# Kernel tuning notes

Hardware: AMD Instinct MI355X
Metric: run time of the kernel (lower is better)

The kernel has to match this reference:

```python
import jax, jax.numpy as jnp
import numpy as np

EPS = 1e-6
DIM, HEADS, HEAD_DIM, FFN = 1024, 16, 64, 4096
B, S = 2, 2048


def layer_norm(x, g, b):
    m = jnp.mean(x, axis=-1, keepdims=True)
    v = jnp.mean(jnp.square(x - m), axis=-1, keepdims=True)
    return (x - m) * jax.lax.rsqrt(v + EPS) * g + b


def apply_rope(x, cos, sin):
    # x: (b, h, s, d); cos/sin: (s, d) broadcast over b, h
    x1, x2 = jnp.split(x, 2, axis=-1)
    rot = jnp.concatenate([-x2, x1], axis=-1)
    return x * cos + rot * sin


def setup_inputs() -> dict:
    key = jax.random.key(0)
    ks = jax.random.split(key, 24)
    sc_in = 1.0 / np.sqrt(DIM)
    sc_ffn = 1.0 / np.sqrt(FFN)
    inp = {
        "x": jax.random.normal(ks[0], (B, S, DIM), jnp.float32),
        "rope_cos": jax.random.uniform(ks[1], (S, HEAD_DIM), jnp.float32),
        "rope_sin": jax.random.uniform(ks[2], (S, HEAD_DIM), jnp.float32),
        "w_qkv": jax.random.normal(ks[3], (3 * DIM, DIM), jnp.float32) * sc_in,
        "b_qkv": jnp.zeros((3 * DIM,), jnp.float32),
        "w_out": jax.random.normal(ks[4], (DIM, DIM), jnp.float32) * sc_in,
        "b_out": jnp.zeros((DIM,), jnp.float32),
        "qn_g": jnp.ones((DIM,), jnp.float32),
        "qn_b": jnp.zeros((DIM,), jnp.float32),
        "kn_g": jnp.ones((DIM,), jnp.float32),
        "kn_b": jnp.zeros((DIM,), jnp.float32),
        "ln1_g": jnp.ones((DIM,), jnp.float32),
        "ln1_b": jnp.zeros((DIM,), jnp.float32),
        "ln2_g": jnp.ones((DIM,), jnp.float32),
        "ln2_b": jnp.zeros((DIM,), jnp.float32),
        "w1": jax.random.normal(ks[5], (FFN, DIM), jnp.float32) * sc_in,
        "b1": jnp.zeros((FFN,), jnp.float32),
        "w2": jax.random.normal(ks[6], (DIM, FFN), jnp.float32) * sc_ffn,
        "b2": jnp.zeros((DIM,), jnp.float32),
        "w3": jax.random.normal(ks[7], (FFN, DIM), jnp.float32) * sc_in,
        "b3": jnp.zeros((FFN,), jnp.float32),
    }
    return inp


def reference(x, rope_cos, rope_sin, w_qkv, b_qkv, w_out, b_out,
              qn_g, qn_b, kn_g, kn_b, ln1_g, ln1_b, ln2_g, ln2_b,
              w1, b1, w2, b2, w3, b3):
    bs, s, d = x.shape
    # --- pre-norm self-attention ---
    h = layer_norm(x, ln1_g, ln1_b)
    qkv = h @ w_qkv.T + b_qkv                      # (b, s, 3d)
    q, k, v = jnp.split(qkv, 3, axis=-1)
    q = layer_norm(q, qn_g, qn_b)                  # QK-norm over full dim
    k = layer_norm(k, kn_g, kn_b)
    # (b, s, d) -> (b, h, s, hd)
    q = q.reshape(bs, s, HEADS, HEAD_DIM).transpose(0, 2, 1, 3)
    k = k.reshape(bs, s, HEADS, HEAD_DIM).transpose(0, 2, 1, 3)
    v = v.reshape(bs, s, HEADS, HEAD_DIM).transpose(0, 2, 1, 3)
    q = apply_rope(q, rope_cos, rope_sin)
    k = apply_rope(k, rope_cos, rope_sin)
    scale = 1.0 / np.sqrt(HEAD_DIM)
    scores = jnp.einsum('bhqd,bhkd->bhqk', q, k) * scale
    probs = jax.nn.softmax(scores, axis=-1)
    attn = jnp.einsum('bhqk,bhkd->bhqd', probs, v)
    attn = attn.transpose(0, 2, 1, 3).reshape(bs, s, d)
    x = x + (attn @ w_out.T + b_out)
    # --- pre-norm SwiGLU FFN ---
    h2 = layer_norm(x, ln2_g, ln2_b)
    ffn = (jax.nn.silu(h2 @ w1.T + b1) * (h2 @ w3.T + b3)) @ w2.T + b2
    return x + ffn
```

## Files before the change

kernel.cpp:

```cpp
#include <hip/hip_runtime.h>
#include <hip/hip_bf16.h>


typedef __bf16 bf16_t;
typedef bf16_t bf16x8 __attribute__((ext_vector_type(8)));
typedef bf16_t bf16x4 __attribute__((ext_vector_type(4)));
typedef float  f32x4  __attribute__((ext_vector_type(4)));
typedef float  f32x16 __attribute__((ext_vector_type(16)));

#define DIM   1024
#define HEADS 16
#define HD    64
#define FFND  4096
#define NB    2
#define SEQ   2048
#define NTOK  (NB * SEQ)

#define GLOAD16(gp, lp) __builtin_amdgcn_global_load_lds( \
    (const __attribute__((address_space(1))) void*)(gp),  \
    (__attribute__((address_space(3))) void*)(lp), 16, 0, 0)

#define CVTPK(lo, hi_) ({ unsigned r_;                                        \
  asm("v_cvt_pk_bf16_f32 %0, %1, %2" : "=v"(r_) : "v"(lo), "v"(hi_)); r_; })
#define PLSWAP(a, b) asm("v_permlane32_swap_b32 %0, %1" : "+v"(a), "+v"(b))

#define F2B_S0 786432
#define F2B_S1 262144
#define F2B_S2 1048576
#define F2B_S3 1048576
#define F2B_S4 1048576
#define F2B_C1 (F2B_S0)
#define F2B_C2 (F2B_C1 + F2B_S1)
#define F2B_C3 (F2B_C2 + F2B_S2)
#define F2B_C4 (F2B_C3 + F2B_S3)
#define F2B_N  (F2B_C4 + F2B_S4)

__global__ void f2bf_all_kernel(const float* __restrict__ s0, const float* __restrict__ s1,
                                const float* __restrict__ s2, const float* __restrict__ s3,
                                const float* __restrict__ s4,
                                bf16_t* __restrict__ d0, bf16_t* __restrict__ d1,
                                bf16_t* __restrict__ d2, bf16_t* __restrict__ d3,
                                bf16_t* __restrict__ d4) {
  int idx = blockIdx.x * blockDim.x + threadIdx.x;
  int stride = gridDim.x * blockDim.x;
  for (; idx < F2B_N; idx += stride) {
    const float* src; bf16_t* dst; int i;
    if (idx < F2B_C1)      { src = s0; dst = d0; i = idx; }
    else if (idx < F2B_C2) { src = s1; dst = d1; i = idx - F2B_C1; }
    else if (idx < F2B_C3) { src = s2; dst = d2; i = idx - F2B_C2; }
    else if (idx < F2B_C4) { src = s3; dst = d3; i = idx - F2B_C3; }
    else                   { src = s4; dst = d4; i = idx - F2B_C4; }
    float4 v = reinterpret_cast<const float4*>(src)[i];
    bf16x4 o;
    o[0] = (bf16_t)v.x; o[1] = (bf16_t)v.y; o[2] = (bf16_t)v.z; o[3] = (bf16_t)v.w;
    reinterpret_cast<bf16x4*>(dst)[i] = o;
  }
}

__global__ __launch_bounds__(256) void ln_kernel(
    const float* __restrict__ x, const float* __restrict__ g,
    const float* __restrict__ b, bf16_t* __restrict__ out) {
  int t = blockIdx.x;
  int i = threadIdx.x;
  float4 v = reinterpret_cast<const float4*>(x + (size_t)t * DIM)[i];
  float s  = v.x + v.y + v.z + v.w;
  float s2 = v.x * v.x + v.y * v.y + v.z * v.z + v.w * v.w;
#pragma unroll
  for (int off = 32; off > 0; off >>= 1) {
    s  += __shfl_down(s, off, 64);
    s2 += __shfl_down(s2, off, 64);
  }
  __shared__ float red[2][4];
  int wid = i >> 6, lane = i & 63;
  if (lane == 0) { red[0][wid] = s; red[1][wid] = s2; }
  __syncthreads();
  float S  = red[0][0] + red[0][1] + red[0][2] + red[0][3];
  float S2 = red[1][0] + red[1][1] + red[1][2] + red[1][3];
  float mean = S * (1.0f / DIM);
  float var  = S2 * (1.0f / DIM) - mean * mean;
  float r = rsqrtf(var + 1e-6f);
  float vv[4] = {v.x, v.y, v.z, v.w};
  bf16x4 o;
#pragma unroll
  for (int j = 0; j < 4; ++j) {
    int d = i * 4 + j;
    o[j] = (bf16_t)((vv[j] - mean) * r * g[d] + b[d]);
  }
  *reinterpret_cast<bf16x4*>(out + (size_t)t * DIM + i * 4) = o;
}

template <int OUT_MODE>
__global__ __launch_bounds__(512, 2) void gemm256(
    const bf16_t* __restrict__ A, const bf16_t* __restrict__ B,
    const float* __restrict__ bias, const bf16_t* __restrict__ comp,
    void* __restrict__ Cout, int M, int N, int Kfull, int Klen) {
  __shared__ __align__(16) bf16_t Al[2][256][64];
  __shared__ __align__(16) bf16_t Bl[2][256][64];
  const int nTn = N >> 8;
  const int nwg = gridDim.x;
  const int bid = blockIdx.x;
  const int swz = ((nwg & 7) == 0) ? ((bid & 7) * (nwg >> 3) + (bid >> 3)) : bid;
  const int bm = swz / nTn, bn = swz % nTn;
  const int k0base = blockIdx.z * Klen;
  const int NT = Klen >> 6;
  const int tid = threadIdx.x, wid = tid >> 6, lane = tid & 63;
  const int wm = wid >> 2, wn = wid & 3;
  const int lr = lane & 15, lg = lane >> 4;
  const int strow = wid * 8 + (lane >> 3);
  const int stg   = ((lane & 7) ^ ((lane >> 3) & 7)) << 3;
  const bf16_t* Abase = A + (size_t)(bm * 256 + strow) * Kfull + k0base + stg;
  const bf16_t* Bbase = B + (size_t)(bn * 256 + strow) * Kfull + k0base + stg;

#define STAGE_A(buf, half, c, t)                                              \
  GLOAD16(Abase + (size_t)((half) * 128 + (c) * 64) * Kfull + (t) * 64,       \
          &Al[buf][(half) * 128 + (c) * 64 + wid * 8][0])
#define STAGE_B(buf, half, c, t)                                              \
  GLOAD16(Bbase + (size_t)((half) * 128 + (c) * 64) * Kfull + (t) * 64,       \
          &Bl[buf][(half) * 128 + (c) * 64 + wid * 8][0])

  f32x4 acc[8][4] = {};
  STAGE_A(0, 0, 0, 0); STAGE_A(0, 0, 1, 0); STAGE_A(0, 1, 0, 0); STAGE_A(0, 1, 1, 0);
  STAGE_B(0, 0, 0, 0); STAGE_B(0, 0, 1, 0); STAGE_B(0, 1, 0, 0); STAGE_B(0, 1, 1, 0);

  for (int t = 0; t < NT; ++t) {
    const int cur = t & 1, nxt = cur ^ 1;
    const bool pf = (t + 1 < NT);
    if (pf) {
      STAGE_A(nxt, 0, 0, t + 1); STAGE_A(nxt, 0, 1, t + 1);
      STAGE_A(nxt, 1, 0, t + 1); STAGE_A(nxt, 1, 1, t + 1);
      asm volatile("s_waitcnt vmcnt(4)");
    } else {
      asm volatile("s_waitcnt vmcnt(0)");
    }
    __builtin_amdgcn_sched_barrier(0);
    __builtin_amdgcn_s_barrier();
    __builtin_amdgcn_sched_barrier(0);
    bf16x8 bfr[4][2], af[2][2];
#pragma unroll
    for (int nf = 0; nf < 4; ++nf)
#pragma unroll
      for (int ks = 0; ks < 2; ++ks) {
        const int row = wn * 64 + nf * 16 + lr;
        const int g = ((ks * 4 + lg) ^ (lane & 7)) << 3;
        bfr[nf][ks] = *reinterpret_cast<const bf16x8*>(&Bl[cur][row][g]);
      }
#pragma unroll
    for (int i = 0; i < 2; ++i)
#pragma unroll
      for (int ks = 0; ks < 2; ++ks) {
        const int row = wm * 128 + i * 16 + lr;
        const int g = ((ks * 4 + lg) ^ (lane & 7)) << 3;
        af[i][ks] = *reinterpret_cast<const bf16x8*>(&Al[cur][row][g]);
      }
    asm volatile("s_waitcnt lgkmcnt(0)");
    __builtin_amdgcn_sched_barrier(0);
    __builtin_amdgcn_s_setprio(1);
#pragma unroll
    for (int i = 0; i < 2; ++i)
#pragma unroll
      for (int nf = 0; nf < 4; ++nf)
#pragma unroll
        for (int ks = 0; ks < 2; ++ks)
          acc[i][nf] = __builtin_amdgcn_mfma_f32_16x16x32_bf16(af[i][ks], bfr[nf][ks], acc[i][nf], 0, 0, 0);
    __builtin_amdgcn_s_setprio(0);
    __builtin_amdgcn_s_barrier();
#pragma unroll
    for (int p = 1; p < 4; ++p) {
#pragma unroll
      for (int i = 0; i < 2; ++i)
#pragma unroll
        for (int ks = 0; ks < 2; ++ks) {
          const int row = wm * 128 + (p * 2 + i) * 16 + lr;
          const int g = ((ks * 4 + lg) ^ (lane & 7)) << 3;
          af[i][ks] = *reinterpret_cast<const bf16x8*>(&Al[cur][row][g]);
        }
      if (p == 1 && pf) {
        STAGE_B(nxt, 0, 0, t + 1); STAGE_B(nxt, 0, 1, t + 1);
        STAGE_B(nxt, 1, 0, t + 1); STAGE_B(nxt, 1, 1, t + 1);
      }
      __builtin_amdgcn_s_barrier();
      asm volatile("s_waitcnt lgkmcnt(0)");
      __builtin_amdgcn_sched_barrier(0);
      __builtin_amdgcn_s_setprio(1);
#pragma unroll
      for (int i = 0; i < 2; ++i)
#pragma unroll
        for (int nf = 0; nf < 4; ++nf)
#pragma unroll
          for (int ks = 0; ks < 2; ++ks)
            acc[p * 2 + i][nf] = __builtin_amdgcn_mfma_f32_16x16x32_bf16(af[i][ks], bfr[nf][ks], acc[p * 2 + i][nf], 0, 0, 0);
      __builtin_amdgcn_s_setprio(0);
      __builtin_amdgcn_s_barrier();
    }
  }
#undef STAGE_A
#undef STAGE_B
  const int r0 = lg * 4;
#pragma unroll
  for (int mf = 0; mf < 8; ++mf) {
#pragma unroll
    for (int r = 0; r < 4; ++r) {
      const int row = bm * 256 + wm * 128 + mf * 16 + r0 + r;
#pragma unroll
      for (int nf = 0; nf < 4; ++nf) {
        const int col = bn * 256 + wn * 64 + nf * 16 + lr;
        float v = acc[mf][nf][r];
        if (OUT_MODE == 1) {
          v += bias[col];
          reinterpret_cast<bf16_t*>(Cout)[(size_t)row * N + col] = (bf16_t)v;
        } else if (OUT_MODE == 2) {
          float* P = reinterpret_cast<float*>(Cout) + (size_t)blockIdx.z * M * N;
          P[(size_t)row * N + col] = v;
        } else {
          v += bias[col];
          float c1 = (float)comp[(size_t)row * N + col];
          float sg = c1 / (1.0f + __expf(-c1));
          reinterpret_cast<bf16_t*>(Cout)[(size_t)row * N + col] = (bf16_t)(sg * v);
        }
      }
    }
  }
}

__global__ void combine_kernel(const float* __restrict__ part,
                               const float* __restrict__ bias,
                               const float* __restrict__ res,
                               float* __restrict__ out, int n4) {
  const int slice = NTOK * DIM / 4;
  int i = blockIdx.x * blockDim.x + threadIdx.x;
  int stride = gridDim.x * blockDim.x;
  const float4* p = reinterpret_cast<const float4*>(part);
  const float4* r4 = reinterpret_cast<const float4*>(res);
  const float4* b4 = reinterpret_cast<const float4*>(bias);
  float4* o4 = reinterpret_cast<float4*>(out);
  for (; i < n4; i += stride) {
    float4 a = p[i], b = p[i + slice], c = p[i + 2 * slice], d = p[i + 3 * slice];
    float4 rr = r4[i];
    float4 bb = b4[i & 255];
    float4 o;
    o.x = a.x + b.x + c.x + d.x + bb.x + rr.x;
    o.y = a.y + b.y + c.y + d.y + bb.y + rr.y;
    o.z = a.z + b.z + c.z + d.z + bb.z + rr.z;
    o.w = a.w + b.w + c.w + d.w + bb.w + rr.w;
    o4[i] = o;
  }
}

template <int OUT_BF16, int HAS_RES>
__global__ __launch_bounds__(256) void gemm_bt(
    const bf16_t* __restrict__ A, const bf16_t* __restrict__ B,
    const float* __restrict__ bias, const float* __restrict__ res,
    void* __restrict__ Cout, int M, int N, int K) {
  __shared__ bf16_t As[128][32];
  __shared__ bf16_t Bs[128][32];
  const int nTn = N >> 7;
  const int bm = blockIdx.x / nTn;
  const int bn = blockIdx.x % nTn;
  const int tid  = threadIdx.x;
  const int wid  = tid >> 6;
  const int lane = tid & 63;
  const int wm = (wid >> 1) * 64, wn = (wid & 1) * 64;
  const int lr = lane & 15;
  const int gq = lane >> 4;
  const int sr = lane >> 2;
  const int sg = lane & 3;
  const int cS = ((sg ^ ((sr >> 1) & 3)) << 3);
  const int swg = ((gq ^ ((lr >> 1) & 3)) << 3);
  f32x4 acc[4][4] = {};
  const bf16_t* Ag0 = A + (size_t)(bm * 128 + wid * 16 + sr) * K + cS;
  const bf16_t* Ag1 = Ag0 + (size_t)64 * K;
  const bf16_t* Bg0 = B + (size_t)(bn * 128 + wid * 16 + sr) * K + cS;
  const bf16_t* Bg1 = Bg0 + (size_t)64 * K;
  bf16_t* ldsA0 = &As[wid * 16][0];
  bf16_t* ldsA1 = &As[64 + wid * 16][0];
  bf16_t* ldsB0 = &Bs[wid * 16][0];
  bf16_t* ldsB1 = &Bs[64 + wid * 16][0];
  for (int k0 = 0; k0 < K; k0 += 32) {
    __syncthreads();
    GLOAD16(Ag0 + k0, ldsA0);
    GLOAD16(Ag1 + k0, ldsA1);
    GLOAD16(Bg0 + k0, ldsB0);
    GLOAD16(Bg1 + k0, ldsB1);
    __syncthreads();
    bf16x8 af[4], bfr[4];
#pragma unroll
    for (int mi = 0; mi < 4; ++mi)
      af[mi] = *reinterpret_cast<const bf16x8*>(&As[wm + mi * 16 + lr][swg]);
#pragma unroll
    for (int ni = 0; ni < 4; ++ni)
      bfr[ni] = *reinterpret_cast<const bf16x8*>(&Bs[wn + ni * 16 + lr][swg]);
#pragma unroll
    for (int mi = 0; mi < 4; ++mi)
#pragma unroll
      for (int ni = 0; ni < 4; ++ni)
        acc[mi][ni] = __builtin_amdgcn_mfma_f32_16x16x32_bf16(af[mi], bfr[ni], acc[mi][ni], 0, 0, 0);
  }
  const int r0 = (lane >> 4) * 4;
#pragma unroll
  for (int mi = 0; mi < 4; ++mi) {
#pragma unroll
    for (int r = 0; r < 4; ++r) {
      int row = bm * 128 + wm + mi * 16 + r0 + r;
#pragma unroll
      for (int ni = 0; ni < 4; ++ni) {
        int col = bn * 128 + wn + ni * 16 + lr;
        float v = acc[mi][ni][r] + bias[col];
        if (HAS_RES) v += res[(size_t)row * N + col];
        if (OUT_BF16)
          reinterpret_cast<bf16_t*>(Cout)[(size_t)row * N + col] = (bf16_t)v;
        else
          reinterpret_cast<float*>(Cout)[(size_t)row * N + col] = v;
      }
    }
  }
}

__global__ __launch_bounds__(256) void qknorm_rope_kernel(
    const bf16_t* __restrict__ qkv,
    const float* __restrict__ qg, const float* __restrict__ qb,
    const float* __restrict__ kg, const float* __restrict__ kb,
    const float* __restrict__ rc, const float* __restrict__ rs,
    bf16_t* __restrict__ q_r, bf16_t* __restrict__ k_r) {
  int t = blockIdx.x;
  int b = t >> 11, s = t & 2047;
  const bf16_t* p = qkv + (size_t)t * 3072;
  int i = threadIdx.x;
  bf16x4 qv = *reinterpret_cast<const bf16x4*>(p + i * 4);
  bf16x4 kv = *reinterpret_cast<const bf16x4*>(p + 1024 + i * 4);
  float q4[4], k4[4];
  float sq = 0.f, sq2 = 0.f, sk = 0.f, sk2 = 0.f;
#pragma unroll
  for (int j = 0; j < 4; ++j) {
    q4[j] = (float)qv[j]; k4[j] = (float)kv[j];
    sq += q4[j]; sq2 += q4[j] * q4[j];
    sk += k4[j]; sk2 += k4[j] * k4[j];
  }
#pragma unroll
  for (int off = 32; off > 0; off >>= 1) {
    sq  += __shfl_down(sq, off, 64);
    sq2 += __shfl_down(sq2, off, 64);
    sk  += __shfl_down(sk, off, 64);
    sk2 += __shfl_down(sk2, off, 64);
  }
  __shared__ float red[4][4];
  int wid = i >> 6, lane = i & 63;
  if (lane == 0) { red[0][wid] = sq; red[1][wid] = sq2; red[2][wid] = sk; red[3][wid] = sk2; }
  __syncthreads();
  float Sq  = red[0][0] + red[0][1] + red[0][2] + red[0][3];
  float Sq2 = red[1][0] + red[1][1] + red[1][2] + red[1][3];
  float Sk  = red[2][0] + red[2][1] + red[2][2] + red[2][3];
  float Sk2 = red[3][0] + red[3][1] + red[3][2] + red[3][3];
  float mq = Sq * (1.0f / DIM);
  float vq = Sq2 * (1.0f / DIM) - mq * mq;
  float rq = rsqrtf(vq + 1e-6f);
  float mk = Sk * (1.0f / DIM);
  float vk = Sk2 * (1.0f / DIM) - mk * mk;
  float rk = rsqrtf(vk + 1e-6f);
  const float QS = 0.18033688011f;
#pragma unroll
  for (int j = 0; j < 4; ++j) {
    int d = i * 4 + j, h = d >> 6, hd = d & 63, dp = d ^ 32;
    float c  = rc[s * HD + hd];
    float sn = rs[s * HD + hd];
    float qn  = (q4[j] - mq) * rq * qg[d] + qb[d];
    float qpn = ((float)p[dp] - mq) * rq * qg[dp] + qb[dp];
    float qo  = qn * c + ((hd < 32) ? -qpn : qpn) * sn;
    float kn  = (k4[j] - mk) * rk * kg[d] + kb[d];
    float kpn = ((float)p[1024 + dp] - mk) * rk * kg[dp] + kb[dp];
    float ko  = kn * c + ((hd < 32) ? -kpn : kpn) * sn;
    size_t oi = ((size_t)(b * HEADS + h) * SEQ + s) * HD + hd;
    q_r[oi] = (bf16_t)(qo * QS);
    k_r[oi] = (bf16_t)ko;
  }
}

__global__ __launch_bounds__(256) void vtrans_kernel(
    const bf16_t* __restrict__ qkv, bf16_t* __restrict__ v_t) {
  __shared__ bf16_t T[64][72];
  const int st = blockIdx.x;
  const int bh = blockIdx.y;
  const int b = bh >> 4, h = bh & 15;
  const int tid = threadIdx.x;
  const int r = tid >> 2, c = (tid & 3) * 8;
  const bf16_t* src = qkv + (size_t)(b * SEQ + st * 64 + r) * 3072 + 2048 + h * 64;
  *reinterpret_cast<bf16x8*>(&T[r][c])      = *reinterpret_cast<const bf16x8*>(src + c);
  *reinterpret_cast<bf16x8*>(&T[r][c + 32]) = *reinterpret_cast<const bf16x8*>(src + c + 32);
  __syncthreads();
  bf16x8 o0, o1;
#pragma unroll
  for (int j = 0; j < 8; ++j) { o0[j] = T[c + j][r]; o1[j] = T[c + 32 + j][r]; }
  bf16_t* dst = v_t + ((size_t)bh * 64 + r) * SEQ + st * 64;
  *reinterpret_cast<bf16x8*>(dst + c)      = o0;
  *reinterpret_cast<bf16x8*>(dst + c + 32) = o1;
}

__global__ __launch_bounds__(256) void attn_kernel(
    const bf16_t* __restrict__ q_r, const bf16_t* __restrict__ k_r,
    const bf16_t* __restrict__ v_t, bf16_t* __restrict__ attn_out) {
  __shared__ __align__(16) bf16_t Ks[2][4096];
  __shared__ __align__(16) bf16_t Vs[2][4096];
  const int bid = blockIdx.x;
  const int hh = bid & 31;
  const int qt = bid >> 5;
  const int bidx = hh >> 4, h = hh & 15;
  const bf16_t* Qp = q_r + (size_t)hh * SEQ * HD;
  const bf16_t* Kp = k_r + (size_t)hh * SEQ * HD;
  const bf16_t* Vp = v_t + (size_t)hh * HD * SEQ;
  const int tid = threadIdx.x, wid = tid >> 6, lane = tid & 63;
  const int lq = lane & 31, hi = lane >> 5;
  const int qA = qt * 256 + wid * 64 + lq;
  const int qB = qA + 32;
  bf16x8 qfA[4], qfB[4];
#pragma unroll
  for (int kdt = 0; kdt < 4; ++kdt) {
    qfA[kdt] = *reinterpret_cast<const bf16x8*>(Qp + (size_t)qA * HD + kdt * 16 + hi * 8);
    qfB[kdt] = *reinterpret_cast<const bf16x8*>(Qp + (size_t)qB * HD + kdt * 16 + hi * 8);
  }
  f32x16 oA0 = {}, oA1 = {}, oB0 = {}, oB1 = {};
  float lA = 0.f, lB = 0.f;
  const int kSrcA = lane * HD + wid * 8;
  const int kSrcB = lane * HD + (wid + 4) * 8;
  const int vSrcA = lane * SEQ + wid * 8;
  const int vSrcB = lane * SEQ + (wid + 4) * 8;
  const int ldsA = wid * 512;
  const int ldsB = 2048 + wid * 512;
  GLOAD16(Kp + kSrcA, &Ks[0][ldsA]);
  GLOAD16(Kp + kSrcB, &Ks[0][ldsB]);
  GLOAD16(Vp + vSrcA, &Vs[0][ldsA]);
  GLOAD16(Vp + vSrcB, &Vs[0][ldsB]);
  __syncthreads();
  for (int kt = 0; kt < SEQ / 64; ++kt) {
    const int cur = kt & 1, nxt = cur ^ 1;
    if (kt + 1 < SEQ / 64) {
      GLOAD16(Kp + (kt + 1) * (64 * HD) + kSrcA, &Ks[nxt][ldsA]);
      GLOAD16(Kp + (kt + 1) * (64 * HD) + kSrcB, &Ks[nxt][ldsB]);
      GLOAD16(Vp + (kt + 1) * 64 + vSrcA, &Vs[nxt][ldsA]);
      GLOAD16(Vp + (kt + 1) * 64 + vSrcB, &Vs[nxt][ldsB]);
    }
    f32x16 sA0 = {}, sA1 = {}, sB0 = {}, sB1 = {};
#pragma unroll
    for (int kdt = 0; kdt < 4; ++kdt) {
      const int goff = (kdt * 2 + hi) * 512;
      bf16x8 kf0 = *reinterpret_cast<const bf16x8*>(&Ks[cur][goff + lq * 8]);
      bf16x8 kf1 = *reinterpret_cast<const bf16x8*>(&Ks[cur][goff + (lq + 32) * 8]);
      sA0 = __builtin_amdgcn_mfma_f32_32x32x16_bf16(kf0, qfA[kdt], sA0, 0, 0, 0);
      sA1 = __builtin_amdgcn_mfma_f32_32x32x16_bf16(kf1, qfA[kdt], sA1, 0, 0, 0);
      sB0 = __builtin_amdgcn_mfma_f32_32x32x16_bf16(kf0, qfB[kdt], sB0, 0, 0, 0);
      sB1 = __builtin_amdgcn_mfma_f32_32x32x16_bf16(kf1, qfB[kdt], sB1, 0, 0, 0);
    }
#pragma unroll
    for (int i = 0; i < 16; ++i) sA0[i] = __builtin_amdgcn_exp2f(sA0[i]);
#pragma unroll
    for (int i = 0; i < 16; ++i) sA1[i] = __builtin_amdgcn_exp2f(sA1[i]);
#pragma unroll
    for (int i = 0; i < 16; ++i) sB0[i] = __builtin_amdgcn_exp2f(sB0[i]);
#pragma unroll
    for (int i = 0; i < 16; ++i) sB1[i] = __builtin_amdgcn_exp2f(sB1[i]);
    {
      f32x16 t = sA0 + sA1;
      float a = ((t[0] + t[8]) + (t[4] + t[12])) + ((t[2] + t[10]) + (t[6] + t[14]));
      float b = ((t[1] + t[9]) + (t[5] + t[13])) + ((t[3] + t[11]) + (t[7] + t[15]));
      lA += a + b;
      f32x16 u = sB0 + sB1;
      float c = ((u[0] + u[8]) + (u[4] + u[12])) + ((u[2] + u[10]) + (u[6] + u[14]));
      float d = ((u[1] + u[9]) + (u[5] + u[13])) + ((u[3] + u[11]) + (u[7] + u[15]));
      lB += c + d;
    }
#pragma unroll
    for (int tt = 0; tt < 2; ++tt) {
#pragma unroll
      for (int ks = 0; ks < 2; ++ks) {
        const f32x16& pA = tt ? sA1 : sA0;
        const f32x16& pB = tt ? sB1 : sB0;
        unsigned a0, b0, c0, d0, a1, b1, c1, d1;
        if (ks == 0) {
          a0 = CVTPK(pA[0], pA[1]); b0 = CVTPK(pA[4], pA[5]);
          c0 = CVTPK(pA[2], pA[3]); d0 = CVTPK(pA[6], pA[7]);
          a1 = CVTPK(pB[0], pB[1]); b1 = CVTPK(pB[4], pB[5]);
          c1 = CVTPK(pB[2], pB[3]); d1 = CVTPK(pB[6], pB[7]);
        } else {
          a0 = CVTPK(pA[8], pA[9]);   b0 = CVTPK(pA[12], pA[13]);
          c0 = CVTPK(pA[10], pA[11]); d0 = CVTPK(pA[14], pA[15]);
          a1 = CVTPK(pB[8], pB[9]);   b1 = CVTPK(pB[12], pB[13]);
          c1 = CVTPK(pB[10], pB[11]); d1 = CVTPK(pB[14], pB[15]);
        }
        PLSWAP(a0, b0); PLSWAP(c0, d0); PLSWAP(a1, b1); PLSWAP(c1, d1);
        union { unsigned u[4]; bf16x8 v; } pfA, pfB;
        pfA.u[0] = a0; pfA.u[1] = c0; pfA.u[2] = b0; pfA.u[3] = d0;
        pfB.u[0] = a1; pfB.u[1] = c1; pfB.u[2] = b1; pfB.u[3] = d1;
        const int gv = (tt * 4 + ks * 2 + hi) * 512;
        bf16x8 vf0 = *reinterpret_cast<const bf16x8*>(&Vs[cur][gv + lq * 8]);
        bf16x8 vf1 = *reinterpret_cast<const bf16x8*>(&Vs[cur][gv + (lq + 32) * 8]);
        oA0 = __builtin_amdgcn_mfma_f32_32x32x16_bf16(vf0, pfA.v, oA0, 0, 0, 0);
        oA1 = __builtin_amdgcn_mfma_f32_32x32x16_bf16(vf1, pfA.v, oA1, 0, 0, 0);
        oB0 = __builtin_amdgcn_mfma_f32_32x32x16_bf16(vf0, pfB.v, oB0, 0, 0, 0);
        oB1 = __builtin_amdgcn_mfma_f32_32x32x16_bf16(vf1, pfB.v, oB1, 0, 0, 0);
      }
    }
    __syncthreads();
  }
  lA += __shfl_xor(lA, 32, 64);
  lB += __shfl_xor(lB, 32, 64);
  float invA = 1.0f / lA;
  float invB = 1.0f / lB;
  bf16_t* orowA = attn_out + ((size_t)(bidx * SEQ + qA)) * DIM + h * 64;
  bf16_t* orowB = attn_out + ((size_t)(bidx * SEQ + qB)) * DIM + h * 64;
#pragma unroll
  for (int g = 0; g < 4; ++g) {
    bf16x4 wA0, wA1, wB0, wB1;
#pragma unroll
    for (int j = 0; j < 4; ++j) {
      wA0[j] = (bf16_t)(oA0[g * 4 + j] * invA);
      wA1[j] = (bf16_t)(oA1[g * 4 + j] * invA);
      wB0[j] = (bf16_t)(oB0[g * 4 + j] * invB);
      wB1[j] = (bf16_t)(oB1[g * 4 + j] * invB);
    }
    *reinterpret_cast<bf16x4*>(orowA + g * 8 + 4 * hi)      = wA0;
    *reinterpret_cast<bf16x4*>(orowA + 32 + g * 8 + 4 * hi) = wA1;
    *reinterpret_cast<bf16x4*>(orowB + g * 8 + 4 * hi)      = wB0;
    *reinterpret_cast<bf16x4*>(orowB + 32 + g * 8 + 4 * hi) = wB1;
  }
}

extern "C" void kernel_launch(void* const* d_in, const int* in_sizes, int n_in,
                              void* d_out, int out_size, void* d_ws, size_t ws_size,
                              hipStream_t stream) {
  const float* x        = (const float*)d_in[0];
  const float* rope_cos = (const float*)d_in[1];
  const float* rope_sin = (const float*)d_in[2];
  const float* w_qkv    = (const float*)d_in[3];
  const float* b_qkv    = (const float*)d_in[4];
  const float* w_out    = (const float*)d_in[5];
  const float* b_out    = (const float*)d_in[6];
  const float* qn_g     = (const float*)d_in[7];
  const float* qn_b     = (const float*)d_in[8];
  const float* kn_g     = (const float*)d_in[9];
  const float* kn_b     = (const float*)d_in[10];
  const float* ln1_g    = (const float*)d_in[11];
  const float* ln1_b    = (const float*)d_in[12];
  const float* ln2_g    = (const float*)d_in[13];
  const float* ln2_b    = (const float*)d_in[14];
  const float* w1       = (const float*)d_in[15];
  const float* b1       = (const float*)d_in[16];
  const float* w2       = (const float*)d_in[17];
  const float* b2       = (const float*)d_in[18];
  const float* w3       = (const float*)d_in[19];
  const float* b3       = (const float*)d_in[20];

  const size_t OFF_WQKV = 0;
  const size_t OFF_WOUT = 6291456;
  const size_t OFF_W1   = 8388608;
  const size_t OFF_W2   = 16777216;
  const size_t OFF_W3   = 25165824;
  const size_t OFF_H1   = 33554432;
  const size_t OFF_QKV  = 41943040;
  const size_t OFF_QR   = 67108864;
  const size_t OFF_KR   = 75497472;
  const size_t OFF_VT   = 83886080;
  const size_t OFF_ATT  = 92274688;
  const size_t OFF_X2   = 100663296;
  const size_t OFF_H2   = 117440512;
  const size_t OFF_A1   = 33554432;
  const size_t OFF_A3   = 67108864;
  const size_t OFF_PART = 125829120;
  const size_t NEEDED   = 125829120;
  const size_t NEED_SPLIT = OFF_PART + 67108864;
  if (ws_size < NEEDED) return;
  const bool use_split = (ws_size >= NEED_SPLIT);

  char* ws = (char*)d_ws;
  bf16_t* wqkv_bf = (bf16_t*)(ws + OFF_WQKV);
  bf16_t* wout_bf = (bf16_t*)(ws + OFF_WOUT);
  bf16_t* w1_bf   = (bf16_t*)(ws + OFF_W1);
  bf16_t* w2_bf   = (bf16_t*)(ws + OFF_W2);
  bf16_t* w3_bf   = (bf16_t*)(ws + OFF_W3);
  bf16_t* h1      = (bf16_t*)(ws + OFF_H1);
  bf16_t* qkv     = (bf16_t*)(ws + OFF_QKV);
  bf16_t* q_r     = (bf16_t*)(ws + OFF_QR);
  bf16_t* k_r     = (bf16_t*)(ws + OFF_KR);
  bf16_t* v_t     = (bf16_t*)(ws + OFF_VT);
  bf16_t* att     = (bf16_t*)(ws + OFF_ATT);
  float*  x2      = (float*)(ws + OFF_X2);
  bf16_t* h2      = (bf16_t*)(ws + OFF_H2);
  bf16_t* a1      = (bf16_t*)(ws + OFF_A1);
  bf16_t* a3      = (bf16_t*)(ws + OFF_A3);
  float*  part    = (float*)(ws + OFF_PART);
  float*  out     = (float*)d_out;

  f2bf_all_kernel<<<2048, 256, 0, stream>>>(w_qkv, w_out, w1, w2, w3,
                                            wqkv_bf, wout_bf, w1_bf, w2_bf, w3_bf);
  ln_kernel<<<NTOK, 256, 0, stream>>>(x, ln1_g, ln1_b, h1);
  gemm256<1><<<dim3(192, 1, 1), 512, 0, stream>>>(h1, wqkv_bf, b_qkv, nullptr, qkv,
                                                  NTOK, 3072, DIM, DIM);
  qknorm_rope_kernel<<<NTOK, 256, 0, stream>>>(qkv, qn_g, qn_b, kn_g, kn_b,
                                               rope_cos, rope_sin, q_r, k_r);
  vtrans_kernel<<<dim3(SEQ / 64, NB * HEADS), 256, 0, stream>>>(qkv, v_t);
  attn_kernel<<<256, 256, 0, stream>>>(q_r, k_r, v_t, att);
  gemm_bt<0, 1><<<32 * 8, 256, 0, stream>>>(att, wout_bf, b_out, x, x2, NTOK, DIM, DIM);
  ln_kernel<<<NTOK, 256, 0, stream>>>(x2, ln2_g, ln2_b, h2);
  gemm256<1><<<dim3(256, 1, 1), 512, 0, stream>>>(h2, w1_bf, b1, nullptr, a1,
                                                  NTOK, FFND, DIM, DIM);
  gemm256<3><<<dim3(256, 1, 1), 512, 0, stream>>>(h2, w3_bf, b3, a1, a3,
                                                  NTOK, FFND, DIM, DIM);
  if (use_split) {
    gemm256<2><<<dim3(64, 1, 4), 512, 0, stream>>>(a3, w2_bf, nullptr, nullptr, part,
                                                   NTOK, DIM, FFND, FFND / 4);
    combine_kernel<<<2048, 256, 0, stream>>>(part, b2, x2, out, NTOK * DIM / 4);
  } else {
    gemm_bt<0, 1><<<32 * 8, 256, 0, stream>>>(a3, w2_bf, b2, x2, out, NTOK, DIM, FFND);
  }
}
```

Baseline: 344.1 us.

## Split attention KV sequence across two wave groups per block and merge in LDS

Doubles the attention block to 512 threads, where each half of the waves processes half of the key/value sequence for the same query tile, then combines the partial outputs and row sums through shared memory before normalizing. The grid stays at 256 blocks, so this is meant to put more waves per CU and shorten each block's serial KV loop. The cost is extra LDS (a larger buffer reused for the exchange), a final barrier and reduction, and higher register pressure under the new launch bounds. The softmax has no running max, so summing the partials directly stays exact.

```diff
diff --git a/kernel.cpp b/kernel.cpp
--- a/kernel.cpp
+++ b/kernel.cpp
@@ -394,22 +394,27 @@
   *reinterpret_cast<bf16x8*>(dst + c + 32) = o1;
 }
 
-__global__ __launch_bounds__(256) void attn_kernel(
+__global__ __launch_bounds__(512, 2) void attn_kernel(
     const bf16_t* __restrict__ q_r, const bf16_t* __restrict__ k_r,
     const bf16_t* __restrict__ v_t, bf16_t* __restrict__ attn_out) {
-  __shared__ __align__(16) bf16_t Ks[2][4096];
-  __shared__ __align__(16) bf16_t Vs[2][4096];
+  __shared__ __align__(16) char smem[69632];
+  bf16_t* KsB = (bf16_t*)smem;
+  bf16_t* VsB = (bf16_t*)(smem + 32768);
+  float*  Xch = (float*)smem;
   const int bid = blockIdx.x;
   const int hh = bid & 31;
   const int qt = bid >> 5;
   const int bidx = hh >> 4, h = hh & 15;
+  const int tid = threadIdx.x, wid = tid >> 6, lane = tid & 63;
+  const int kh = wid >> 2, ww = wid & 3;
+  const int lq = lane & 31, hi = lane >> 5;
+  const int qA = qt * 256 + ww * 64 + lq;
+  const int qB = qA + 32;
   const bf16_t* Qp = q_r + (size_t)hh * SEQ * HD;
-  const bf16_t* Kp = k_r + (size_t)hh * SEQ * HD;
-  const bf16_t* Vp = v_t + (size_t)hh * HD * SEQ;
-  const int tid = threadIdx.x, wid = tid >> 6, lane = tid & 63;
-  const int lq = lane & 31, hi = lane >> 5;
-  const int qA = qt * 256 + wid * 64 + lq;
-  const int qB = qA + 32;
+  const bf16_t* Kp = k_r + (size_t)hh * SEQ * HD + (size_t)kh * 1024 * HD;
+  const bf16_t* Vp = v_t + (size_t)hh * HD * SEQ + kh * 1024;
+  bf16_t* Ks0 = KsB + kh * 2 * 4096;
+  bf16_t* Vs0 = VsB + kh * 2 * 4096;
   bf16x8 qfA[4], qfB[4];
 #pragma unroll
   for (int kdt = 0; kdt < 4; ++kdt) {
@@ -418,31 +423,32 @@
   }
   f32x16 oA0 = {}, oA1 = {}, oB0 = {}, oB1 = {};
   float lA = 0.f, lB = 0.f;
-  const int kSrcA = lane * HD + wid * 8;
-  const int kSrcB = lane * HD + (wid + 4) * 8;
-  const int vSrcA = lane * SEQ + wid * 8;
-  const int vSrcB = lane * SEQ + (wid + 4) * 8;
-  const int ldsA = wid * 512;
-  const int ldsB = 2048 + wid * 512;
-  GLOAD16(Kp + kSrcA, &Ks[0][ldsA]);
-  GLOAD16(Kp + kSrcB, &Ks[0][ldsB]);
-  GLOAD16(Vp + vSrcA, &Vs[0][ldsA]);
-  GLOAD16(Vp + vSrcB, &Vs[0][ldsB]);
+  const int kSrcA = lane * HD + ww * 8;
+  const int kSrcB = lane * HD + (ww + 4) * 8;
+  const int vSrcA = lane * SEQ + ww * 8;
+  const int vSrcB = lane * SEQ + (ww + 4) * 8;
+  const int ldsA = ww * 512;
+  const int ldsB = 2048 + ww * 512;
+  GLOAD16(Kp + kSrcA, &Ks0[ldsA]);
+  GLOAD16(Kp + kSrcB, &Ks0[ldsB]);
+  GLOAD16(Vp + vSrcA, &Vs0[ldsA]);
+  GLOAD16(Vp + vSrcB, &Vs0[ldsB]);
   __syncthreads();
-  for (int kt = 0; kt < SEQ / 64; ++kt) {
+  const int NT = 1024 / 64;
+  for (int kt = 0; kt < NT; ++kt) {
     const int cur = kt & 1, nxt = cur ^ 1;
-    if (kt + 1 < SEQ / 64) {
-      GLOAD16(Kp + (kt + 1) * (64 * HD) + kSrcA, &Ks[nxt][ldsA]);
-      GLOAD16(Kp + (kt + 1) * (64 * HD) + kSrcB, &Ks[nxt][ldsB]);
-      GLOAD16(Vp + (kt + 1) * 64 + vSrcA, &Vs[nxt][ldsA]);
-      GLOAD16(Vp + (kt + 1) * 64 + vSrcB, &Vs[nxt][ldsB]);
+    if (kt + 1 < NT) {
+      GLOAD16(Kp + (kt + 1) * (64 * HD) + kSrcA, &Ks0[nxt * 4096 + ldsA]);
+      GLOAD16(Kp + (kt + 1) * (64 * HD) + kSrcB, &Ks0[nxt * 4096 + ldsB]);
+      GLOAD16(Vp + (kt + 1) * 64 + vSrcA, &Vs0[nxt * 4096 + ldsA]);
+      GLOAD16(Vp + (kt + 1) * 64 + vSrcB, &Vs0[nxt * 4096 + ldsB]);
     }
     f32x16 sA0 = {}, sA1 = {}, sB0 = {}, sB1 = {};
 #pragma unroll
     for (int kdt = 0; kdt < 4; ++kdt) {
-      const int goff = (kdt * 2 + hi) * 512;
-      bf16x8 kf0 = *reinterpret_cast<const bf16x8*>(&Ks[cur][goff + lq * 8]);
-      bf16x8 kf1 = *reinterpret_cast<const bf16x8*>(&Ks[cur][goff + (lq + 32) * 8]);
+      const int goff = cur * 4096 + (kdt * 2 + hi) * 512;
+      bf16x8 kf0 = *reinterpret_cast<const bf16x8*>(&Ks0[goff + lq * 8]);
+      bf16x8 kf1 = *reinterpret_cast<const bf16x8*>(&Ks0[goff + (lq + 32) * 8]);
       sA0 = __builtin_amdgcn_mfma_f32_32x32x16_bf16(kf0, qfA[kdt], sA0, 0, 0, 0);
       sA1 = __builtin_amdgcn_mfma_f32_32x32x16_bf16(kf1, qfA[kdt], sA1, 0, 0, 0);
       sB0 = __builtin_amdgcn_mfma_f32_32x32x16_bf16(kf0, qfB[kdt], sB0, 0, 0, 0);
@@ -488,9 +494,9 @@
         union { unsigned u[4]; bf16x8 v; } pfA, pfB;
         pfA.u[0] = a0; pfA.u[1] = c0; pfA.u[2] = b0; pfA.u[3] = d0;
         pfB.u[0] = a1; pfB.u[1] = c1; pfB.u[2] = b1; pfB.u[3] = d1;
-        const int gv = (tt * 4 + ks * 2 + hi) * 512;
-        bf16x8 vf0 = *reinterpret_cast<const bf16x8*>(&Vs[cur][gv + lq * 8]);
-        bf16x8 vf1 = *reinterpret_cast<const bf16x8*>(&Vs[cur][gv + (lq + 32) * 8]);
+        const int gv = cur * 4096 + (tt * 4 + ks * 2 + hi) * 512;
+        bf16x8 vf0 = *reinterpret_cast<const bf16x8*>(&Vs0[gv + lq * 8]);
+        bf16x8 vf1 = *reinterpret_cast<const bf16x8*>(&Vs0[gv + (lq + 32) * 8]);
         oA0 = __builtin_amdgcn_mfma_f32_32x32x16_bf16(vf0, pfA.v, oA0, 0, 0, 0);
         oA1 = __builtin_amdgcn_mfma_f32_32x32x16_bf16(vf1, pfA.v, oA1, 0, 0, 0);
         oB0 = __builtin_amdgcn_mfma_f32_32x32x16_bf16(vf0, pfB.v, oB0, 0, 0, 0);
@@ -501,24 +507,44 @@
   }
   lA += __shfl_xor(lA, 32, 64);
   lB += __shfl_xor(lB, 32, 64);
-  float invA = 1.0f / lA;
-  float invB = 1.0f / lB;
-  bf16_t* orowA = attn_out + ((size_t)(bidx * SEQ + qA)) * DIM + h * 64;
-  bf16_t* orowB = attn_out + ((size_t)(bidx * SEQ + qB)) * DIM + h * 64;
-#pragma unroll
-  for (int g = 0; g < 4; ++g) {
-    bf16x4 wA0, wA1, wB0, wB1;
-#pragma unroll
-    for (int j = 0; j < 4; ++j) {
-      wA0[j] = (bf16_t)(oA0[g * 4 + j] * invA);
-      wA1[j] = (bf16_t)(oA1[g * 4 + j] * invA);
-      wB0[j] = (bf16_t)(oB0[g * 4 + j] * invB);
-      wB1[j] = (bf16_t)(oB1[g * 4 + j] * invB);
-    }
-    *reinterpret_cast<bf16x4*>(orowA + g * 8 + 4 * hi)      = wA0;
-    *reinterpret_cast<bf16x4*>(orowA + 32 + g * 8 + 4 * hi) = wA1;
-    *reinterpret_cast<bf16x4*>(orowB + g * 8 + 4 * hi)      = wB0;
-    *reinterpret_cast<bf16x4*>(orowB + 32 + g * 8 + 4 * hi) = wB1;
+  if (kh == 1) {
+    float* my = Xch + (size_t)(ww * 64 + lane) * 68;
+#pragma unroll
+    for (int g = 0; g < 4; ++g) {
+      *reinterpret_cast<float4*>(my + g * 4)      = make_float4(oA0[g*4], oA0[g*4+1], oA0[g*4+2], oA0[g*4+3]);
+      *reinterpret_cast<float4*>(my + 16 + g * 4) = make_float4(oA1[g*4], oA1[g*4+1], oA1[g*4+2], oA1[g*4+3]);
+      *reinterpret_cast<float4*>(my + 32 + g * 4) = make_float4(oB0[g*4], oB0[g*4+1], oB0[g*4+2], oB0[g*4+3]);
+      *reinterpret_cast<float4*>(my + 48 + g * 4) = make_float4(oB1[g*4], oB1[g*4+1], oB1[g*4+2], oB1[g*4+3]);
+    }
+    my[64] = lA; my[65] = lB;
+  }
+  __syncthreads();
+  if (kh == 0) {
+    const float* pr = Xch + (size_t)(ww * 64 + lane) * 68;
+#pragma unroll
+    for (int i = 0; i < 16; ++i) {
+      oA0[i] += pr[i];      oA1[i] += pr[16 + i];
+      oB0[i] += pr[32 + i]; oB1[i] += pr[48 + i];
+    }
+    float invA = 1.0f / (lA + pr[64]);
+    float invB = 1.0f / (lB + pr[65]);
+    bf16_t* orowA = attn_out + ((size_t)(bidx * SEQ + qA)) * DIM + h * 64;
+    bf16_t* orowB = attn_out + ((size_t)(bidx * SEQ + qB)) * DIM + h * 64;
+#pragma unroll
+    for (int g = 0; g < 4; ++g) {
+      bf16x4 wA0, wA1, wB0, wB1;
+#pragma unroll
+      for (int j = 0; j < 4; ++j) {
+        wA0[j] = (bf16_t)(oA0[g * 4 + j] * invA);
+        wA1[j] = (bf16_t)(oA1[g * 4 + j] * invA);
+        wB0[j] = (bf16_t)(oB0[g * 4 + j] * invB);
+        wB1[j] = (bf16_t)(oB1[g * 4 + j] * invB);
+      }
+      *reinterpret_cast<bf16x4*>(orowA + g * 8 + 4 * hi)      = wA0;
+      *reinterpret_cast<bf16x4*>(orowA + 32 + g * 8 + 4 * hi) = wA1;
+      *reinterpret_cast<bf16x4*>(orowB + g * 8 + 4 * hi)      = wB0;
+      *reinterpret_cast<bf16x4*>(orowB + 32 + g * 8 + 4 * hi) = wB1;
+    }
   }
 }
 
@@ -595,7 +621,7 @@
   qknorm_rope_kernel<<<NTOK, 256, 0, stream>>>(qkv, qn_g, qn_b, kn_g, kn_b,
                                                rope_cos, rope_sin, q_r, k_r);
   vtrans_kernel<<<dim3(SEQ / 64, NB * HEADS), 256, 0, stream>>>(qkv, v_t);
-  attn_kernel<<<256, 256, 0, stream>>>(q_r, k_r, v_t, att);
+  attn_kernel<<<256, 512, 0, stream>>>(q_r, k_r, v_t, att);
   gemm_bt<0, 1><<<32 * 8, 256, 0, stream>>>(att, wout_bf, b_out, x, x2, NTOK, DIM, DIM);
   ln_kernel<<<NTOK, 256, 0, stream>>>(x2, ln2_g, ln2_b, h2);
   gemm256<1><<<dim3(256, 1, 1), 512, 0, stream>>>(h2, w1_bf, b1, nullptr, a1,
```

Result: faster. 321.0 us (-6.7%).
